# Performance work log

Measured on AMD Instinct MI355X. Metric: run time of the kernel, lower is better.

Reference implementation:

```python
import jax, jax.numpy as jnp
import numpy as np

SCALE, K, PATCH, STRIDE = 2, 5, 3, 1
EPS = 1e-5


def im2patch(x, p, s):
    # x: (b,c,H,W) -> (b,c,p,p,m1,m2), 'VALID' patches (padding is 0 for our sizes)
    b, c, H, W = x.shape
    m1 = (H - p) // s + 1
    m2 = (W - p) // s + 1
    ii = (jnp.arange(m1) * s)[:, None] + jnp.arange(p)[None, :]   # (m1,p)
    jj = (jnp.arange(m2) * s)[:, None] + jnp.arange(p)[None, :]   # (m2,p)
    pt = x[:, :, ii[:, :, None, None], jj[None, None, :, :]]      # (b,c,m1,p,m2,p)
    return pt.transpose(0, 1, 3, 5, 2, 4)                         # (b,c,p,p,m1,m2)


def patch2im(patches, p, s):
    # overlap-add fold, averaged by per-pixel patch counts (torch F.fold / ones-fold divisor)
    b, c, _, _, m1, m2 = patches.shape
    Hp = (m1 - 1) * s + p
    Wp = (m2 - 1) * s + p
    out = jnp.zeros((b, c, Hp, Wp), patches.dtype)
    cnt = jnp.zeros((Hp, Wp), patches.dtype)
    for i in range(p):          # fixed small loop over patch offsets (p*p = 36)
        for j in range(p):
            out = out.at[:, :, i:i + s * m1:s, j:j + s * m2:s].add(patches[:, :, i, j])
            cnt = cnt.at[i:i + s * m1:s, j:j + s * m2:s].add(1.0)
    return out / cnt


def setup_inputs():
    key = jax.random.key(0)
    k1, k2, k3 = jax.random.split(key, 3)
    b, cy, H, W = 1, 64, 80, 80
    y = jax.random.normal(k1, (b, cy, H, W), jnp.float32)
    yd = jax.random.normal(k2, (b, cy * SCALE ** 2, H // SCALE, W // SCALE), jnp.float32)
    m = ((H - PATCH) // STRIDE + 1) ** 2
    n = ((H // SCALE - PATCH) // STRIDE + 1) ** 2
    idx_k = jax.random.randint(k3, (b, m, K), 0, n, jnp.int32)
    return {"y": y, "yd": yd, "idx_k": idx_k}


def reference(y, yd, idx_k):
    b, cy, H, W = y.shape
    c = yd.shape[1]           # = cy * scale^2
    rs = SCALE ** 2
    y_p = im2patch(y, PATCH, STRIDE)      # (b,cy,p,p,m1,m2)
    yd_p = im2patch(yd, PATCH, STRIDE)    # (b,c,p,p,n1,n2)
    m1, m2 = y_p.shape[-2:]
    n1, n2 = yd_p.shape[-2:]
    m, n = m1 * m2, n1 * n2
    f = c * PATCH * PATCH
    y_flat = y_p.transpose(0, 4, 5, 1, 2, 3).reshape(b, m, f // rs)
    yd_flat = yd_p.transpose(0, 4, 5, 1, 2, 3).reshape(b, n, f)
    # top-k neighbor gather: (b,n,f)[idx (b,m,k)] -> (b,m,k,f) -> (b,m,f,k)
    z = jax.vmap(lambda t, i: t[i])(yd_flat, idx_k)
    z = z.transpose(0, 1, 3, 2)
    # AdaIN: normalize gathered HR patches, apply LR query patch stats (unbiased var, torch default)
    y_n = y_flat.reshape(b, m, c // rs, PATCH * PATCH)
    z_n = z.reshape(b, m, c // rs, rs * PATCH * PATCH, K)
    z_mu = z_n.mean(axis=3, keepdims=True)
    z_sd = jnp.sqrt(z_n.var(axis=3, ddof=1, keepdims=True) + EPS)
    y_mu = y_n.mean(axis=3, keepdims=True)[..., None]        # (b,m,c',1,1)
    y_sd = jnp.sqrt(y_n.var(axis=3, ddof=1, keepdims=True) + EPS)[..., None]
    z = ((z_n - z_mu) / z_sd * y_sd + y_mu).reshape(b, m, f, K)
    # rearrange f = (cy, scale, scale, p1, p2) into SR patches (b, k*cy, p*scale, p*scale, m1, m2)
    z = z.transpose(0, 3, 2, 1)                                   # (b,k,f,m)
    z = z.reshape(b, K, cy, SCALE, SCALE, PATCH, PATCH, m1, m2)
    z = z.transpose(0, 1, 2, 5, 3, 6, 4, 7, 8)                    # (b,k,cy,p1,s,p2,s,m1,m2)
    z = z.reshape(b, K * cy, PATCH * SCALE, PATCH * SCALE, m1, m2)
    z_sr = patch2im(z, PATCH * SCALE, STRIDE * SCALE)             # (b,k*cy,H*scale,W*scale)
    return z_sr.reshape(b, K * cy, H * SCALE, W * SCALE)
```

## Files before the change

kernel.cpp:

```cpp
#include <hip/hip_runtime.h>
#include <hip/hip_fp16.h>
#include <string.h>

#define CY     64
#define HY     80
#define HD     40
#define SPD    (HD*HD)
#define M1     78
#define N1     38
#define M_TOT  (M1*M1)
#define N_TOT  (N1*N1)
#define KK     5
#define HS     160
#define EPSF   1e-5f
#define LP     33

typedef float f32x2 __attribute__((ext_vector_type(2)));

__device__ __forceinline__ unsigned pkf16(float a, float b) {
    __half2 h = __floats2half2_rn(a, b);
    unsigned u; memcpy(&u, &h, 4); return u;
}
__device__ __forceinline__ f32x2 upk2(unsigned u) {
    __half2 h; memcpy(&h, &u, 4);
    float2 f = __half22float2(h);
    f32x2 r; r.x = f.x; r.y = f.y; return r;
}

__global__ __launch_bounds__(256) void pre_kernel(const float* __restrict__ y,
                                                  const float* __restrict__ yd,
                                                  uint4* __restrict__ ydW,
                                                  unsigned* __restrict__ zstP,
                                                  unsigned* __restrict__ ystP) {
    int id = blockIdx.x * 256 + threadIdx.x;
    if (id < SPD * 64) {
        int cc = id & 63, sp = id >> 6;
        const float* b0 = yd + (cc * 4) * SPD + sp;
        int d = (sp < SPD - 1) ? 1 : 0;
        ydW[sp * 64 + cc] = make_uint4(pkf16(b0[0], b0[SPD]),
                                       pkf16(b0[2*SPD], b0[3*SPD]),
                                       pkf16(b0[d], b0[SPD+d]),
                                       pkf16(b0[2*SPD+d], b0[3*SPD+d]));
        return;
    }
    id -= SPD * 64;
    if (id < N_TOT * 64) {
        int n  = id % N_TOT;
        int cc = id / N_TOT;
        int ni = n / N1, nj = n - ni * N1;
        const float* base = yd + (cc * 4) * SPD + ni * HD + nj;
        float s = 0.f, sq = 0.f;
#pragma unroll
        for (int r = 0; r < 4; ++r)
#pragma unroll
            for (int i = 0; i < 3; ++i)
#pragma unroll
                for (int j = 0; j < 3; ++j) {
                    float v = base[r * SPD + i * HD + j];
                    s += v; sq += v * v;
                }
        float mu  = s * (1.f / 36.f);
        float var = (sq - 36.f * mu * mu) * (1.f / 35.f);
        zstP[n * 64 + cc] = pkf16(mu, rsqrtf(var + EPSF));
        return;
    }
    id -= N_TOT * 64;
    if (id >= CY * M_TOT) return;
    int m  = id % M_TOT;
    int cc = id / M_TOT;
    int mi = m / M1, mj = m - mi * M1;
    const float* base = y + cc * (HY * HY) + mi * HY + mj;
    float s = 0.f, sq = 0.f;
#pragma unroll
    for (int i = 0; i < 3; ++i)
#pragma unroll
        for (int j = 0; j < 3; ++j) {
            float v = base[i * HY + j];
            s += v; sq += v * v;
        }
    float mu  = s * (1.f / 9.f);
    float var = (sq - 9.f * mu * mu) * (1.f / 8.f);
    ystP[m * 64 + cc] = pkf16(mu, sqrtf(var + EPSF));
}

__global__ __launch_bounds__(512) void agg_kernel(
    const uint4* __restrict__ ydW, const unsigned* __restrict__ zstP,
    const unsigned* __restrict__ ystP, const int* __restrict__ idx,
    float* __restrict__ out)
{
    __shared__ float lds[128 * LP];

    int lane = threadIdx.x & 63;
    int w    = __builtin_amdgcn_readfirstlane(threadIdx.x >> 6);
    int bid  = blockIdx.x;
    int wg   = (bid & 7) * 250 + (bid >> 3);
    int k    = wg / 400;
    int rem  = wg - k * 400;
    int y    = rem / 5;
    int xb2  = rem - y * 5;
    int x0   = xb2 * 16 + w * 2;

    f32x2 acc01[2] = {{0.f,0.f},{0.f,0.f}};
    f32x2 acc23[2] = {{0.f,0.f},{0.f,0.f}};
    float bs[2] = {0.f, 0.f};
    float inv0, inv1;

    auto serve = [&](f32x2& a01, f32x2& a23, float& bsum,
                     unsigned lo, unsigned hi, float a, float b) {
        f32x2 am; am.x = a; am.y = a;
        a01 = __builtin_elementwise_fma(am, upk2(lo), a01);
        a23 = __builtin_elementwise_fma(am, upk2(hi), a23);
        bsum += b;
    };

    if (y >= 2 && y <= M1 - 1 && x0 >= 2 && x0 <= M1 - 2) {
        inv0 = inv1 = 1.f / 9.f;
        unsigned ysu[12], zsu[12];
        int nn[12];
#pragma unroll
        for (int p = 0; p < 12; ++p) {
            int m = (y - 2 + (p >> 2)) * M1 + (x0 - 2 + (p & 3));
            nn[p]  = idx[m * KK + k];
            ysu[p] = ystP[m * 64 + lane];
        }
#pragma unroll
        for (int p = 0; p < 12; ++p)
            zsu[p] = zstP[nn[p] * 64 + lane];
        float aa[12], bb[12];
        int spb[12];
#pragma unroll
        for (int p = 0; p < 12; ++p) {
            f32x2 ys = upk2(ysu[p]), zs = upk2(zsu[p]);
            aa[p] = ys.y * zs.y;
            bb[p] = fmaf(-zs.x, aa[p], ys.x);
            int n = nn[p], ni = n / N1;
            spb[p] = ni * HD + (n - ni * N1);
        }
#pragma unroll
        for (int r = 0; r < 3; ++r) {
            int roff = (2 - r) * HD;
            int s0 = spb[r*4+0] + roff, s1 = spb[r*4+1] + roff;
            int s2 = spb[r*4+2] + roff, s3 = spb[r*4+3] + roff;
            uint2 v0 = *(const uint2*)(ydW + (s0 + 2) * 64 + lane);
            uint4 v1 = ydW[(s1 + 1) * 64 + lane];
            uint4 v2 = ydW[(s2 + 0) * 64 + lane];
            uint2 v3 = *(const uint2*)(ydW + (s3 + 0) * 64 + lane);
            serve(acc01[0], acc23[0], bs[0], v0.x, v0.y, aa[r*4+0], bb[r*4+0]);
            serve(acc01[0], acc23[0], bs[0], v1.x, v1.y, aa[r*4+1], bb[r*4+1]);
            serve(acc01[1], acc23[1], bs[1], v1.z, v1.w, aa[r*4+1], bb[r*4+1]);
            serve(acc01[0], acc23[0], bs[0], v2.x, v2.y, aa[r*4+2], bb[r*4+2]);
            serve(acc01[1], acc23[1], bs[1], v2.z, v2.w, aa[r*4+2], bb[r*4+2]);
            serve(acc01[1], acc23[1], bs[1], v3.x, v3.y, aa[r*4+3], bb[r*4+3]);
        }
    } else {
#pragma unroll
        for (int q = 0; q < 2; ++q) {
            int x = x0 + q;
            int milo = max(0, y - 2), mihi = min(M1 - 1, y);
            int mjlo = max(0, x - 2), mjhi = min(M1 - 1, x);
            float iv = 1.f / (float)((mihi - milo + 1) * (mjhi - mjlo + 1));
            if (q == 0) inv0 = iv; else inv1 = iv;
            for (int mi = milo; mi <= mihi; ++mi)
                for (int mj = mjlo; mj <= mjhi; ++mj) {
                    int m = mi * M1 + mj;
                    int n = idx[m * KK + k];
                    f32x2 ys = upk2(ystP[m * 64 + lane]);
                    f32x2 zs = upk2(zstP[n * 64 + lane]);
                    float a = ys.y * zs.y;
                    float b = fmaf(-zs.x, a, ys.x);
                    int ni = n / N1;
                    int sp = ni * HD + (n - ni * N1) + (y - mi) * HD + (x - mj);
                    uint2 v = *(const uint2*)(ydW + sp * 64 + lane);
                    if (q == 0) serve(acc01[0], acc23[0], bs[0], v.x, v.y, a, b);
                    else        serve(acc01[1], acc23[1], bs[1], v.x, v.y, a, b);
                }
        }
    }

#pragma unroll
    for (int q = 0; q < 2; ++q) {
        float iv = q ? inv1 : inv0;
        float bq = bs[q];
        int col = (w * 2 + q) * 2;
        lds[(0 * CY + lane) * LP + col]     = (acc01[q].x + bq) * iv;
        lds[(0 * CY + lane) * LP + col + 1] = (acc01[q].y + bq) * iv;
        lds[(1 * CY + lane) * LP + col]     = (acc23[q].x + bq) * iv;
        lds[(1 * CY + lane) * LP + col + 1] = (acc23[q].y + bq) * iv;
    }

    __syncthreads();

    int rsel = lane >> 5, c = lane & 31;
    int X0 = xb2 * 32, Y0 = 2 * y;
#pragma unroll
    for (int t = 0; t < 8; ++t) {
        int row = t * 16 + w * 2 + rsel;
        float v = lds[row * LP + c];
        int dy = row >> 6, cc = row & 63;
        __builtin_nontemporal_store(v,
            out + (((size_t)(k * CY + cc) * HS + (Y0 + dy)) * HS + X0 + c));
    }
}

extern "C" void kernel_launch(void* const* d_in, const int* in_sizes, int n_in,
                              void* d_out, int out_size, void* d_ws, size_t ws_size,
                              hipStream_t stream) {
    const float* y   = (const float*)d_in[0];
    const float* yd  = (const float*)d_in[1];
    const int*   idx = (const int*)d_in[2];
    float* out = (float*)d_out;

    char* ws = (char*)d_ws;
    uint4*    ydW  = (uint4*)ws;
    unsigned* zstP = (unsigned*)(ws + 1638400);
    unsigned* ystP = (unsigned*)(ws + 2008064);

    int pre_total = SPD * 64 + N_TOT * 64 + CY * M_TOT;
    pre_kernel<<<(pre_total + 255) / 256, 256, 0, stream>>>(y, yd, ydW, zstP, ystP);
    agg_kernel<<<KK * 400, 512, 0, stream>>>(ydW, zstP, ystP, idx, out);
}
```

Before: 34.74 us.

## Cooperatively precompute per-patch AdaIN coefficients into LDS shared by all waves

Each workgroup now first computes the AdaIN scale/shift coefficients and neighbor offsets for its 3x18 window of query patches into shared memory, with all 512 threads cooperating. Interior waves then read these from LDS instead of each recomputing 12 idx/ystP/zstP loads, which removes the redundant overlapping patch work between adjacent waves. The cost is an extra prologue phase, an added barrier, and LDS reuse that needs another sync. The boundary path still computes its coefficients directly.

After: 36.33 us. +4.6%, slower.

```diff
diff --git a/kernel.cpp b/kernel.cpp
--- a/kernel.cpp
+++ b/kernel.cpp
@@ -14,6 +14,7 @@
 #define HS     160
 #define EPSF   1e-5f
 #define LP     33
+#define NU     54
 
 typedef float f32x2 __attribute__((ext_vector_type(2)));
 
@@ -88,7 +89,7 @@
     const unsigned* __restrict__ ystP, const int* __restrict__ idx,
     float* __restrict__ out)
 {
-    __shared__ float lds[128 * LP];
+    __shared__ unsigned lds_u[128 * LP];
 
     int lane = threadIdx.x & 63;
     int w    = __builtin_amdgcn_readfirstlane(threadIdx.x >> 6);
@@ -100,42 +101,45 @@
     int xb2  = rem - y * 5;
     int x0   = xb2 * 16 + w * 2;
 
+    int row0 = y - 2, col0 = xb2 * 16 - 2;
+    for (int t = threadIdx.x; t < NU * 64; t += 512) {
+        int cc = t & 63, u = t >> 6;
+        int mi = row0 + u / 18, mj = col0 + u % 18;
+        if (mi >= 0 && mi < M1 && mj >= 0 && mj < M1) {
+            int m = mi * M1 + mj;
+            int n = idx[m * KK + k];
+            f32x2 ys = upk2(ystP[m * 64 + cc]);
+            f32x2 zs = upk2(zstP[n * 64 + cc]);
+            float a = ys.y * zs.y;
+            float b = fmaf(-zs.x, a, ys.x);
+            lds_u[u * 64 + cc] = pkf16(a, b);
+            if (cc == 0) {
+                int ni = n / N1;
+                lds_u[NU * 64 + u] = (unsigned)(ni * HD + (n - ni * N1));
+            }
+        }
+    }
+    __syncthreads();
+
     f32x2 acc01[2] = {{0.f,0.f},{0.f,0.f}};
     f32x2 acc23[2] = {{0.f,0.f},{0.f,0.f}};
     float bs[2] = {0.f, 0.f};
     float inv0, inv1;
 
-    auto serve = [&](f32x2& a01, f32x2& a23, float& bsum,
-                     unsigned lo, unsigned hi, float a, float b) {
+    auto serve = [&](int q, unsigned lo, unsigned hi, float a, float b) {
         f32x2 am; am.x = a; am.y = a;
-        a01 = __builtin_elementwise_fma(am, upk2(lo), a01);
-        a23 = __builtin_elementwise_fma(am, upk2(hi), a23);
-        bsum += b;
+        acc01[q] = __builtin_elementwise_fma(am, upk2(lo), acc01[q]);
+        acc23[q] = __builtin_elementwise_fma(am, upk2(hi), acc23[q]);
+        bs[q] += b;
     };
 
     if (y >= 2 && y <= M1 - 1 && x0 >= 2 && x0 <= M1 - 2) {
         inv0 = inv1 = 1.f / 9.f;
-        unsigned ysu[12], zsu[12];
-        int nn[12];
-#pragma unroll
-        for (int p = 0; p < 12; ++p) {
-            int m = (y - 2 + (p >> 2)) * M1 + (x0 - 2 + (p & 3));
-            nn[p]  = idx[m * KK + k];
-            ysu[p] = ystP[m * 64 + lane];
-        }
+        int spb[12];
 #pragma unroll
         for (int p = 0; p < 12; ++p)
-            zsu[p] = zstP[nn[p] * 64 + lane];
-        float aa[12], bb[12];
-        int spb[12];
-#pragma unroll
-        for (int p = 0; p < 12; ++p) {
-            f32x2 ys = upk2(ysu[p]), zs = upk2(zsu[p]);
-            aa[p] = ys.y * zs.y;
-            bb[p] = fmaf(-zs.x, aa[p], ys.x);
-            int n = nn[p], ni = n / N1;
-            spb[p] = ni * HD + (n - ni * N1);
-        }
+            spb[p] = __builtin_amdgcn_readfirstlane(
+                        (int)lds_u[NU * 64 + (p >> 2) * 18 + w * 2 + (p & 3)]);
 #pragma unroll
         for (int r = 0; r < 3; ++r) {
             int roff = (2 - r) * HD;
@@ -145,12 +149,17 @@
             uint4 v1 = ydW[(s1 + 1) * 64 + lane];
             uint4 v2 = ydW[(s2 + 0) * 64 + lane];
             uint2 v3 = *(const uint2*)(ydW + (s3 + 0) * 64 + lane);
-            serve(acc01[0], acc23[0], bs[0], v0.x, v0.y, aa[r*4+0], bb[r*4+0]);
-            serve(acc01[0], acc23[0], bs[0], v1.x, v1.y, aa[r*4+1], bb[r*4+1]);
-            serve(acc01[1], acc23[1], bs[1], v1.z, v1.w, aa[r*4+1], bb[r*4+1]);
-            serve(acc01[0], acc23[0], bs[0], v2.x, v2.y, aa[r*4+2], bb[r*4+2]);
-            serve(acc01[1], acc23[1], bs[1], v2.z, v2.w, aa[r*4+2], bb[r*4+2]);
-            serve(acc01[1], acc23[1], bs[1], v3.x, v3.y, aa[r*4+3], bb[r*4+3]);
+            int ub = (r * 18 + w * 2) * 64 + lane;
+            f32x2 c0 = upk2(lds_u[ub]);
+            f32x2 c1 = upk2(lds_u[ub + 64]);
+            f32x2 c2 = upk2(lds_u[ub + 128]);
+            f32x2 c3 = upk2(lds_u[ub + 192]);
+            serve(0, v0.x, v0.y, c0.x, c0.y);
+            serve(0, v1.x, v1.y, c1.x, c1.y);
+            serve(1, v1.z, v1.w, c1.x, c1.y);
+            serve(0, v2.x, v2.y, c2.x, c2.y);
+            serve(1, v2.z, v2.w, c2.x, c2.y);
+            serve(1, v3.x, v3.y, c3.x, c3.y);
         }
     } else {
 #pragma unroll
@@ -171,21 +180,23 @@
                     int ni = n / N1;
                     int sp = ni * HD + (n - ni * N1) + (y - mi) * HD + (x - mj);
                     uint2 v = *(const uint2*)(ydW + sp * 64 + lane);
-                    if (q == 0) serve(acc01[0], acc23[0], bs[0], v.x, v.y, a, b);
-                    else        serve(acc01[1], acc23[1], bs[1], v.x, v.y, a, b);
+                    serve(q, v.x, v.y, a, b);
                 }
         }
     }
 
+    __syncthreads();
+
+    float* ldsf = (float*)lds_u;
 #pragma unroll
     for (int q = 0; q < 2; ++q) {
         float iv = q ? inv1 : inv0;
         float bq = bs[q];
         int col = (w * 2 + q) * 2;
-        lds[(0 * CY + lane) * LP + col]     = (acc01[q].x + bq) * iv;
-        lds[(0 * CY + lane) * LP + col + 1] = (acc01[q].y + bq) * iv;
-        lds[(1 * CY + lane) * LP + col]     = (acc23[q].x + bq) * iv;
-        lds[(1 * CY + lane) * LP + col + 1] = (acc23[q].y + bq) * iv;
+        ldsf[(0 * CY + lane) * LP + col]     = (acc01[q].x + bq) * iv;
+        ldsf[(0 * CY + lane) * LP + col + 1] = (acc01[q].y + bq) * iv;
+        ldsf[(1 * CY + lane) * LP + col]     = (acc23[q].x + bq) * iv;
+        ldsf[(1 * CY + lane) * LP + col + 1] = (acc23[q].y + bq) * iv;
     }
 
     __syncthreads();
@@ -195,7 +206,7 @@
 #pragma unroll
     for (int t = 0; t < 8; ++t) {
         int row = t * 16 + w * 2 + rsel;
-        float v = lds[row * LP + c];
+        float v = ldsf[row * LP + c];
         int dy = row >> 6, cc = row & 63;
         __builtin_nontemporal_store(v,
             out + (((size_t)(k * CY + cc) * HS + (Y0 + dy)) * HS + X0 + c));
```
